# Performance work log

Hardware: AMD Instinct MI355X
Metric: run time of the kernel (lower is better)

Reference implementation:

```python
import jax, jax.numpy as jnp
import numpy as np

d_model = 512


def setup_inputs() -> dict:
    key = jax.random.key(0)
    k1, k2, k3, k4 = jax.random.split(key, 4)
    B, T, d_k = 8, 2048, 64
    scale = 1.0 / np.sqrt(d_model)
    x = jax.random.normal(k1, (B, T, d_model), dtype=jnp.float32)
    Wk = jax.random.normal(k2, (d_model, d_k), dtype=jnp.float32) * scale
    Wq = jax.random.normal(k3, (d_model, d_k), dtype=jnp.float32) * scale
    Wv = jax.random.normal(k4, (d_model, d_k), dtype=jnp.float32) * scale
    return {"x": x, "Wk": Wk, "Wq": Wq, "Wv": Wv}


def reference(x, Wk, Wq, Wv):
    # x: [B,T,C]; W*: [C,d_k]  (torch Linear weight is [d_k,C]; we store transposed)
    k = jnp.einsum('btc,cd->btd', x, Wk)
    q = jnp.einsum('btc,cd->btd', x, Wq)
    v = jnp.einsum('btc,cd->btd', x, Wv)
    d_k = k.shape[-1]
    scores = jnp.einsum('bqd,bkd->bqk', q, k) / jnp.sqrt(jnp.float32(d_k))
    attn = jax.nn.softmax(scores, axis=-1)  # [B,T,T]
    return jnp.einsum('bqk,bkd->bqd', attn, v)
```

## Files before the change

kernel.cpp:

```cpp
#include <hip/hip_runtime.h>
#include <hip/hip_bf16.h>
#include <stdint.h>


typedef short bf16x8 __attribute__((ext_vector_type(8)));
typedef float f32x4 __attribute__((ext_vector_type(4)));

#define MFMA_BF16 __builtin_amdgcn_mfma_f32_16x16x32_bf16

__device__ __forceinline__ unsigned int pk2(float a, float b) {
    __hip_bfloat162 h = __float22bfloat162_rn(float2{a, b});
    union { __hip_bfloat162 h; unsigned int u; } r; r.h = h;
    return r.u;
}

__device__ __forceinline__ uint2 pack4_bf16(float a, float b, float c, float d) {
    uint2 r; r.x = pk2(a, b); r.y = pk2(c, d); return r;
}

__device__ __forceinline__ bf16x8 cvt8(f32x4 a, f32x4 b) {
    union { bf16x8 v; unsigned int u[4]; } r;
    r.u[0] = pk2(a[0], a[1]); r.u[1] = pk2(a[2], a[3]);
    r.u[2] = pk2(b[0], b[1]); r.u[3] = pk2(b[2], b[3]);
    return r.v;
}

__device__ __forceinline__ unsigned short bf1(float a) {
    __hip_bfloat16 h = __float2bfloat16(a);
    union { __hip_bfloat16 h; unsigned short u; } r; r.h = h;
    return r.u;
}

__global__ void wt_kernel(const float* __restrict__ Wq,
                          const float* __restrict__ Wk,
                          const float* __restrict__ Wv,
                          unsigned short* __restrict__ wt2)
{
    int id = blockIdx.x * 256 + threadIdx.x;
    int c    = id & 15;
    int quad = (id >> 4) & 3;
    int ks   = (id >> 6) & 15;
    int mt   = (id >> 10) & 3;
    int w    = id >> 12;
    const float* src = (w == 0) ? Wq : ((w == 1) ? Wk : Wv);
    const int n  = mt * 16 + c;
    const int k0 = ks * 32 + quad * 8;
    unsigned short* dst = wt2 + (size_t)id * 8;
    #pragma unroll
    for (int j = 0; j < 8; j++)
        dst[j] = bf1(src[(size_t)(k0 + j) * 64 + n]);
}

__global__ __launch_bounds__(256, 1) void proj_kernel(
    const float* __restrict__ x, const unsigned short* __restrict__ wt2,
    unsigned short* __restrict__ qg, unsigned short* __restrict__ kg2,
    unsigned short* __restrict__ vg2)
{
    __shared__ unsigned short xs[8192];

    const int tid  = threadIdx.x;
    const int lane = tid & 63;
    const int wave = tid >> 6;
    const int c    = lane & 15;
    const int quad = lane >> 4;
    const int tt   = blockIdx.x;
    const int t0   = tt * 16;

    const float* xb = x + (size_t)tt * 8192;
    #pragma unroll
    for (int t = 0; t < 4; t++) {
        int i = t * 256 + tid;
        f32x4 a = *(const f32x4*)(xb + (size_t)i * 8);
        f32x4 b = *(const f32x4*)(xb + (size_t)i * 8 + 4);
        int tok = i >> 6;
        int db  = i & 63;
        *(bf16x8*)(xs + db * 128 + ((tok ^ (db & 7)) * 8)) = cvt8(a, b);
    }
    __syncthreads();

    f32x4 acc[3];
    #pragma unroll
    for (int r = 0; r < 3; r++) acc[r] = f32x4{0.f, 0.f, 0.f, 0.f};

    const int fbase = wave * 3;
    #pragma unroll 4
    for (int ks = 0; ks < 16; ks++) {
        bf16x8 xf = *(const bf16x8*)(
            xs + ks * 512 + quad * 128 + ((c ^ ((ks * 4 + quad) & 7)) * 8));
        #pragma unroll
        for (int r = 0; r < 3; r++) {
            int f = fbase + r;
            bf16x8 wa = *(const bf16x8*)(wt2 + ((size_t)(f * 16 + ks) * 64 + lane) * 8);
            acc[r] = MFMA_BF16(wa, xf, acc[r], 0, 0, 0);
        }
    }

    const int b  = t0 >> 11;
    const int tb = t0 & 2047;

    #pragma unroll
    for (int r = 0; r < 3; r++) {
        const int f  = fbase + r;
        const int w  = f >> 2;
        const int mt = f & 3;
        if (w == 0) {
            unsigned short* base = qg + (size_t)(t0 + c) * 64;
            *(uint2*)(base + mt * 16 + quad * 4) =
                pack4_bf16(acc[r][0], acc[r][1], acc[r][2], acc[r][3]);
        } else if (w == 1) {
            const int g  = tb >> 4;
            const int h  = mt >> 1;
            const int qk = (mt & 1) * 2 + (quad >> 1);
            size_t chunk = (size_t)b * 16384 + ((size_t)(g * 2 + h) * 4 + qk) * 16 + c;
            *(uint2*)(kg2 + chunk * 8 + (quad & 1) * 4) =
                pack4_bf16(acc[r][0], acc[r][1], acc[r][2], acc[r][3]);
        } else {
            const int tk = tb + c;
            const int s  = tk >> 5;
            const int qv = (tk >> 3) & 3;
            const int j  = tk & 7;
            size_t chunk = (size_t)b * 16384 + ((size_t)(s * 4 + mt) * 4 + qv) * 16 + quad * 4;
            unsigned short* dst = vg2 + chunk * 8 + j;
            dst[0]  = bf1(acc[r][0]);
            dst[8]  = bf1(acc[r][1]);
            dst[16] = bf1(acc[r][2]);
            dst[24] = bf1(acc[r][3]);
        }
    }
}

__global__ __launch_bounds__(512, 2) void attn_kernel(
    const unsigned short* __restrict__ qg, const unsigned short* __restrict__ kg2,
    const unsigned short* __restrict__ vg2, float* __restrict__ out)
{
    __shared__ __align__(16) unsigned short pt[8][4][16 * 136];
    __shared__ float lbuf[8][4][16];
    float* obase = reinterpret_cast<float*>(&pt[0][0][0]);

    const int lane = threadIdx.x & 63;
    const int wave = threadIdx.x >> 6;
    const int c    = lane & 15;
    const int quad = lane >> 4;
    const int b    = blockIdx.x & 7;
    const int g    = blockIdx.x >> 3;
    const int tb   = b * 2048 + g * 64;

    unsigned short* ptw = &pt[wave][0][0];
    const unsigned short* kbase = kg2 + ((size_t)b * 16384 + lane) * 8;
    const unsigned short* vbase = vg2 + ((size_t)b * 16384 + lane) * 8;

    bf16x8 qA0 = *(const bf16x8*)(qg + (size_t)(tb + c) * 64 + quad * 8);
    bf16x8 qA1 = *(const bf16x8*)(qg + (size_t)(tb + c) * 64 + 32 + quad * 8);
    bf16x8 qB0 = *(const bf16x8*)(qg + (size_t)(tb + 16 + c) * 64 + quad * 8);
    bf16x8 qB1 = *(const bf16x8*)(qg + (size_t)(tb + 16 + c) * 64 + 32 + quad * 8);
    bf16x8 qC0 = *(const bf16x8*)(qg + (size_t)(tb + 32 + c) * 64 + quad * 8);
    bf16x8 qC1 = *(const bf16x8*)(qg + (size_t)(tb + 32 + c) * 64 + 32 + quad * 8);
    bf16x8 qD0 = *(const bf16x8*)(qg + (size_t)(tb + 48 + c) * 64 + quad * 8);
    bf16x8 qD1 = *(const bf16x8*)(qg + (size_t)(tb + 48 + c) * 64 + 32 + quad * 8);

    f32x4 oa0 = {0,0,0,0}, oa1 = {0,0,0,0}, oa2 = {0,0,0,0}, oa3 = {0,0,0,0};
    f32x4 ob0 = {0,0,0,0}, ob1 = {0,0,0,0}, ob2 = {0,0,0,0}, ob3 = {0,0,0,0};
    f32x4 oc0 = {0,0,0,0}, oc1 = {0,0,0,0}, oc2 = {0,0,0,0}, oc3 = {0,0,0,0};
    f32x4 od0 = {0,0,0,0}, od1 = {0,0,0,0}, od2 = {0,0,0,0}, od3 = {0,0,0,0};
    f32x4 laccA = {0,0,0,0}, laccB = {0,0,0,0};
    f32x4 laccC = {0,0,0,0}, laccD = {0,0,0,0};
    const float cexp = 0.18033688011112042f;

    for (int kt = wave * 2; kt < wave * 2 + 2; kt++) {
        const int key0 = kt * 128;
        const int g0   = key0 >> 4;
        const int s0   = key0 >> 5;
        const f32x4 z = {0,0,0,0};

        f32x4 stA[8], stB[8];
        #pragma unroll
        for (int mt = 0; mt < 8; mt++) {
            bf16x8 k0 = *(const bf16x8*)(kbase + (size_t)((g0 + mt) * 2    ) * 64 * 8);
            bf16x8 k1 = *(const bf16x8*)(kbase + (size_t)((g0 + mt) * 2 + 1) * 64 * 8);
            stA[mt] = MFMA_BF16(k0, qA0, z, 0, 0, 0);
            stA[mt] = MFMA_BF16(k1, qA1, stA[mt], 0, 0, 0);
            stB[mt] = MFMA_BF16(k0, qB0, z, 0, 0, 0);
            stB[mt] = MFMA_BF16(k1, qB1, stB[mt], 0, 0, 0);
        }

        asm volatile("" ::: "memory");
        #pragma unroll
        for (int mt = 0; mt < 8; mt++) {
            float p0 = __builtin_amdgcn_exp2f(stA[mt][0] * cexp);
            float p1 = __builtin_amdgcn_exp2f(stA[mt][1] * cexp);
            float p2 = __builtin_amdgcn_exp2f(stA[mt][2] * cexp);
            float p3 = __builtin_amdgcn_exp2f(stA[mt][3] * cexp);
            laccA[0] += p0; laccA[1] += p1; laccA[2] += p2; laccA[3] += p3;
            *(uint2*)(ptw + c * 136 + mt * 16 + quad * 4) = pack4_bf16(p0, p1, p2, p3);
        }
        #pragma unroll
        for (int mt = 0; mt < 8; mt++) {
            float p0 = __builtin_amdgcn_exp2f(stB[mt][0] * cexp);
            float p1 = __builtin_amdgcn_exp2f(stB[mt][1] * cexp);
            float p2 = __builtin_amdgcn_exp2f(stB[mt][2] * cexp);
            float p3 = __builtin_amdgcn_exp2f(stB[mt][3] * cexp);
            laccB[0] += p0; laccB[1] += p1; laccB[2] += p2; laccB[3] += p3;
            *(uint2*)(ptw + 2176 + c * 136 + mt * 16 + quad * 4) = pack4_bf16(p0, p1, p2, p3);
        }
        asm volatile("" ::: "memory");

        f32x4 stC[8], stD[8];
        #pragma unroll
        for (int mt = 0; mt < 8; mt++) {
            bf16x8 k0 = *(const bf16x8*)(kbase + (size_t)((g0 + mt) * 2    ) * 64 * 8);
            bf16x8 k1 = *(const bf16x8*)(kbase + (size_t)((g0 + mt) * 2 + 1) * 64 * 8);
            stC[mt] = MFMA_BF16(k0, qC0, z, 0, 0, 0);
            stC[mt] = MFMA_BF16(k1, qC1, stC[mt], 0, 0, 0);
            stD[mt] = MFMA_BF16(k0, qD0, z, 0, 0, 0);
            stD[mt] = MFMA_BF16(k1, qD1, stD[mt], 0, 0, 0);
        }

        bf16x8 va[2][4];
        #pragma unroll
        for (int mt = 0; mt < 4; mt++) {
            va[0][mt] = *(const bf16x8*)(vbase + (size_t)((s0    ) * 4 + mt) * 64 * 8);
            va[1][mt] = *(const bf16x8*)(vbase + (size_t)((s0 + 1) * 4 + mt) * 64 * 8);
        }

        asm volatile("" ::: "memory");
        #pragma unroll
        for (int mt = 0; mt < 8; mt++) {
            float p0 = __builtin_amdgcn_exp2f(stC[mt][0] * cexp);
            float p1 = __builtin_amdgcn_exp2f(stC[mt][1] * cexp);
            float p2 = __builtin_amdgcn_exp2f(stC[mt][2] * cexp);
            float p3 = __builtin_amdgcn_exp2f(stC[mt][3] * cexp);
            laccC[0] += p0; laccC[1] += p1; laccC[2] += p2; laccC[3] += p3;
            *(uint2*)(ptw + 2 * 2176 + c * 136 + mt * 16 + quad * 4) = pack4_bf16(p0, p1, p2, p3);
        }
        #pragma unroll
        for (int mt = 0; mt < 8; mt++) {
            float p0 = __builtin_amdgcn_exp2f(stD[mt][0] * cexp);
            float p1 = __builtin_amdgcn_exp2f(stD[mt][1] * cexp);
            float p2 = __builtin_amdgcn_exp2f(stD[mt][2] * cexp);
            float p3 = __builtin_amdgcn_exp2f(stD[mt][3] * cexp);
            laccD[0] += p0; laccD[1] += p1; laccD[2] += p2; laccD[3] += p3;
            *(uint2*)(ptw + 3 * 2176 + c * 136 + mt * 16 + quad * 4) = pack4_bf16(p0, p1, p2, p3);
        }
        asm volatile("" ::: "memory");

        #pragma unroll
        for (int ks = 0; ks < 4; ks++) {
            bf16x8 pbA = *(const bf16x8*)(ptw            + c * 136 + ks * 32 + quad * 8);
            bf16x8 pbB = *(const bf16x8*)(ptw +     2176 + c * 136 + ks * 32 + quad * 8);
            bf16x8 pbC = *(const bf16x8*)(ptw + 2 * 2176 + c * 136 + ks * 32 + quad * 8);
            bf16x8 pbD = *(const bf16x8*)(ptw + 3 * 2176 + c * 136 + ks * 32 + quad * 8);
            bf16x8 v0 = va[ks & 1][0], v1 = va[ks & 1][1];
            bf16x8 v2 = va[ks & 1][2], v3 = va[ks & 1][3];
            if (ks < 2) {
                #pragma unroll
                for (int mt = 0; mt < 4; mt++)
                    va[ks & 1][mt] =
                        *(const bf16x8*)(vbase + (size_t)((s0 + ks + 2) * 4 + mt) * 64 * 8);
            }
            oa0 = MFMA_BF16(v0, pbA, oa0, 0, 0, 0);
            oa1 = MFMA_BF16(v1, pbA, oa1, 0, 0, 0);
            oa2 = MFMA_BF16(v2, pbA, oa2, 0, 0, 0);
            oa3 = MFMA_BF16(v3, pbA, oa3, 0, 0, 0);
            ob0 = MFMA_BF16(v0, pbB, ob0, 0, 0, 0);
            ob1 = MFMA_BF16(v1, pbB, ob1, 0, 0, 0);
            ob2 = MFMA_BF16(v2, pbB, ob2, 0, 0, 0);
            ob3 = MFMA_BF16(v3, pbB, ob3, 0, 0, 0);
            oc0 = MFMA_BF16(v0, pbC, oc0, 0, 0, 0);
            oc1 = MFMA_BF16(v1, pbC, oc1, 0, 0, 0);
            oc2 = MFMA_BF16(v2, pbC, oc2, 0, 0, 0);
            oc3 = MFMA_BF16(v3, pbC, oc3, 0, 0, 0);
            od0 = MFMA_BF16(v0, pbD, od0, 0, 0, 0);
            od1 = MFMA_BF16(v1, pbD, od1, 0, 0, 0);
            od2 = MFMA_BF16(v2, pbD, od2, 0, 0, 0);
            od3 = MFMA_BF16(v3, pbD, od3, 0, 0, 0);
        }
        asm volatile("" ::: "memory");
    }

    float lA = (laccA[0] + laccA[1]) + (laccA[2] + laccA[3]);
    lA += __shfl_xor(lA, 16); lA += __shfl_xor(lA, 32);
    float lB = (laccB[0] + laccB[1]) + (laccB[2] + laccB[3]);
    lB += __shfl_xor(lB, 16); lB += __shfl_xor(lB, 32);
    float lC = (laccC[0] + laccC[1]) + (laccC[2] + laccC[3]);
    lC += __shfl_xor(lC, 16); lC += __shfl_xor(lC, 32);
    float lD = (laccD[0] + laccD[1]) + (laccD[2] + laccD[3]);
    lD += __shfl_xor(lD, 16); lD += __shfl_xor(lD, 32);
    if (quad == 0) {
        lbuf[wave][0][c] = lA; lbuf[wave][1][c] = lB;
        lbuf[wave][2][c] = lC; lbuf[wave][3][c] = lD;
    }

    __syncthreads();

    if (wave < 4) {
        float* o0 = obase + ((size_t)(wave * 4 + 0) * 16 + c) * 68 + quad * 4;
        float* o1 = obase + ((size_t)(wave * 4 + 1) * 16 + c) * 68 + quad * 4;
        float* o2 = obase + ((size_t)(wave * 4 + 2) * 16 + c) * 68 + quad * 4;
        float* o3 = obase + ((size_t)(wave * 4 + 3) * 16 + c) * 68 + quad * 4;
        *(f32x4*)(o0 +  0) = oa0; *(f32x4*)(o0 + 16) = oa1;
        *(f32x4*)(o0 + 32) = oa2; *(f32x4*)(o0 + 48) = oa3;
        *(f32x4*)(o1 +  0) = ob0; *(f32x4*)(o1 + 16) = ob1;
        *(f32x4*)(o1 + 32) = ob2; *(f32x4*)(o1 + 48) = ob3;
        *(f32x4*)(o2 +  0) = oc0; *(f32x4*)(o2 + 16) = oc1;
        *(f32x4*)(o2 + 32) = oc2; *(f32x4*)(o2 + 48) = oc3;
        *(f32x4*)(o3 +  0) = od0; *(f32x4*)(o3 + 16) = od1;
        *(f32x4*)(o3 + 32) = od2; *(f32x4*)(o3 + 48) = od3;
    }
    __syncthreads();

    if (wave >= 4) {
        const int p = wave - 4;
        float* o0 = obase + ((size_t)(p * 4 + 0) * 16 + c) * 68 + quad * 4;
        float* o1 = obase + ((size_t)(p * 4 + 1) * 16 + c) * 68 + quad * 4;
        float* o2 = obase + ((size_t)(p * 4 + 2) * 16 + c) * 68 + quad * 4;
        float* o3 = obase + ((size_t)(p * 4 + 3) * 16 + c) * 68 + quad * 4;
        #define ADDSTORE(ptr, off, reg) { f32x4 t = *(f32x4*)((ptr) + (off)); \
            t[0] += reg[0]; t[1] += reg[1]; t[2] += reg[2]; t[3] += reg[3];   \
            *(f32x4*)((ptr) + (off)) = t; }
        ADDSTORE(o0,  0, oa0); ADDSTORE(o0, 16, oa1);
        ADDSTORE(o0, 32, oa2); ADDSTORE(o0, 48, oa3);
        ADDSTORE(o1,  0, ob0); ADDSTORE(o1, 16, ob1);
        ADDSTORE(o1, 32, ob2); ADDSTORE(o1, 48, ob3);
        ADDSTORE(o2,  0, oc0); ADDSTORE(o2, 16, oc1);
        ADDSTORE(o2, 32, oc2); ADDSTORE(o2, 48, oc3);
        ADDSTORE(o3,  0, od0); ADDSTORE(o3, 16, od1);
        ADDSTORE(o3, 32, od2); ADDSTORE(o3, 48, od3);
        #undef ADDSTORE
    }
    __syncthreads();

    const int tid = threadIdx.x;
    const int row = tid >> 3;
    const int d0  = (tid & 7) * 8;
    const int qt  = row >> 4;
    const int r   = row & 15;
    float L = 0.f;
    #pragma unroll
    for (int w = 0; w < 8; w++) L += lbuf[w][qt][r];
    const float rl = 1.f / L;
    f32x4 Oa = {0,0,0,0}, Ob = {0,0,0,0};
    #pragma unroll
    for (int p = 0; p < 4; p++) {
        const float* src = obase + ((size_t)(p * 4 + qt) * 16 + r) * 68 + d0;
        f32x4 a   = *(const f32x4*)(src);
        f32x4 bfr = *(const f32x4*)(src + 4);
        Oa[0] += a[0]; Oa[1] += a[1]; Oa[2] += a[2]; Oa[3] += a[3];
        Ob[0] += bfr[0]; Ob[1] += bfr[1]; Ob[2] += bfr[2]; Ob[3] += bfr[3];
    }
    Oa[0] *= rl; Oa[1] *= rl; Oa[2] *= rl; Oa[3] *= rl;
    Ob[0] *= rl; Ob[1] *= rl; Ob[2] *= rl; Ob[3] *= rl;
    float* op = out + (size_t)(tb + row) * 64 + d0;
    *(f32x4*)op       = Oa;
    *(f32x4*)(op + 4) = Ob;
}

extern "C" void kernel_launch(void* const* d_in, const int* in_sizes, int n_in,
                              void* d_out, int out_size, void* d_ws, size_t ws_size,
                              hipStream_t stream)
{
    const float* x  = (const float*)d_in[0];
    const float* Wk = (const float*)d_in[1];
    const float* Wq = (const float*)d_in[2];
    const float* Wv = (const float*)d_in[3];
    float* out = (float*)d_out;

    char* ws = (char*)d_ws;
    unsigned short* qg  = (unsigned short*)(ws);
    unsigned short* kg2 = (unsigned short*)(ws + (2u << 20));
    unsigned short* vg2 = (unsigned short*)(ws + (4u << 20));
    unsigned short* wt2 = (unsigned short*)(ws + (6u << 20));

    hipLaunchKernelGGL(wt_kernel,   dim3(48),   dim3(256), 0, stream,
                       Wq, Wk, Wv, wt2);
    hipLaunchKernelGGL(proj_kernel, dim3(1024), dim3(256), 0, stream,
                       x, wt2, qg, kg2, vg2);
    hipLaunchKernelGGL(attn_kernel, dim3(256),  dim3(512), 0, stream,
                       qg, kg2, vg2, out);
}
```

Measured before the change: 109.3 us.

## Process 64 tokens per projection block to reuse weight fragments across subtiles

The projection kernel now handles 64 tokens per block instead of 16, with four 16-token subtiles per wave. Each weight fragment loaded from global memory is reused across all four subtiles, which cuts repeated weight loads and raises MFMA density. The cost is a 64KB shared-memory staging buffer, four times as many accumulators per thread, and only 256 blocks instead of 1024. That lower block count may leave many compute units underused during the projection.

```diff
diff --git a/kernel.cpp b/kernel.cpp
--- a/kernel.cpp
+++ b/kernel.cpp
@@ -56,7 +56,7 @@
     unsigned short* __restrict__ qg, unsigned short* __restrict__ kg2,
     unsigned short* __restrict__ vg2)
 {
-    __shared__ unsigned short xs[8192];
+    __shared__ unsigned short xs[32768];
 
     const int tid  = threadIdx.x;
     const int lane = tid & 63;
@@ -64,67 +64,79 @@
     const int c    = lane & 15;
     const int quad = lane >> 4;
     const int tt   = blockIdx.x;
-    const int t0   = tt * 16;
-
-    const float* xb = x + (size_t)tt * 8192;
-    #pragma unroll
-    for (int t = 0; t < 4; t++) {
+    const int t0   = tt * 64;
+
+    const float* xb = x + (size_t)tt * 32768;
+    #pragma unroll
+    for (int t = 0; t < 16; t++) {
         int i = t * 256 + tid;
         f32x4 a = *(const f32x4*)(xb + (size_t)i * 8);
         f32x4 b = *(const f32x4*)(xb + (size_t)i * 8 + 4);
         int tok = i >> 6;
         int db  = i & 63;
-        *(bf16x8*)(xs + db * 128 + ((tok ^ (db & 7)) * 8)) = cvt8(a, b);
+        *(bf16x8*)(xs + ((size_t)db * 64 + (tok ^ (db & 7))) * 8) = cvt8(a, b);
     }
     __syncthreads();
 
-    f32x4 acc[3];
-    #pragma unroll
-    for (int r = 0; r < 3; r++) acc[r] = f32x4{0.f, 0.f, 0.f, 0.f};
+    f32x4 acc[3][4];
+    #pragma unroll
+    for (int r = 0; r < 3; r++)
+        #pragma unroll
+        for (int st = 0; st < 4; st++) acc[r][st] = f32x4{0.f, 0.f, 0.f, 0.f};
 
     const int fbase = wave * 3;
-    #pragma unroll 4
+    #pragma unroll 2
     for (int ks = 0; ks < 16; ks++) {
-        bf16x8 xf = *(const bf16x8*)(
-            xs + ks * 512 + quad * 128 + ((c ^ ((ks * 4 + quad) & 7)) * 8));
-        #pragma unroll
-        for (int r = 0; r < 3; r++) {
-            int f = fbase + r;
-            bf16x8 wa = *(const bf16x8*)(wt2 + ((size_t)(f * 16 + ks) * 64 + lane) * 8);
-            acc[r] = MFMA_BF16(wa, xf, acc[r], 0, 0, 0);
-        }
-    }
-
-    const int b  = t0 >> 11;
-    const int tb = t0 & 2047;
+        bf16x8 wa[3];
+        #pragma unroll
+        for (int r = 0; r < 3; r++)
+            wa[r] = *(const bf16x8*)(
+                wt2 + ((size_t)((fbase + r) * 16 + ks) * 64 + lane) * 8);
+        const int sw = c ^ ((ks & 1) * 4 + quad);
+        const unsigned short* xrow = xs + ((size_t)(ks * 4 + quad) * 64 + sw) * 8;
+        #pragma unroll
+        for (int st = 0; st < 4; st++) {
+            bf16x8 xf = *(const bf16x8*)(xrow + (size_t)st * 16 * 8);
+            #pragma unroll
+            for (int r = 0; r < 3; r++)
+                acc[r][st] = MFMA_BF16(wa[r], xf, acc[r][st], 0, 0, 0);
+        }
+    }
+
+    const int b = t0 >> 11;
 
     #pragma unroll
     for (int r = 0; r < 3; r++) {
         const int f  = fbase + r;
         const int w  = f >> 2;
         const int mt = f & 3;
-        if (w == 0) {
-            unsigned short* base = qg + (size_t)(t0 + c) * 64;
-            *(uint2*)(base + mt * 16 + quad * 4) =
-                pack4_bf16(acc[r][0], acc[r][1], acc[r][2], acc[r][3]);
-        } else if (w == 1) {
-            const int g  = tb >> 4;
-            const int h  = mt >> 1;
-            const int qk = (mt & 1) * 2 + (quad >> 1);
-            size_t chunk = (size_t)b * 16384 + ((size_t)(g * 2 + h) * 4 + qk) * 16 + c;
-            *(uint2*)(kg2 + chunk * 8 + (quad & 1) * 4) =
-                pack4_bf16(acc[r][0], acc[r][1], acc[r][2], acc[r][3]);
-        } else {
-            const int tk = tb + c;
-            const int s  = tk >> 5;
-            const int qv = (tk >> 3) & 3;
-            const int j  = tk & 7;
-            size_t chunk = (size_t)b * 16384 + ((size_t)(s * 4 + mt) * 4 + qv) * 16 + quad * 4;
-            unsigned short* dst = vg2 + chunk * 8 + j;
-            dst[0]  = bf1(acc[r][0]);
-            dst[8]  = bf1(acc[r][1]);
-            dst[16] = bf1(acc[r][2]);
-            dst[24] = bf1(acc[r][3]);
+        #pragma unroll
+        for (int st = 0; st < 4; st++) {
+            const int ts = t0 + st * 16;
+            const int tb = ts & 2047;
+            if (w == 0) {
+                unsigned short* base = qg + (size_t)(ts + c) * 64;
+                *(uint2*)(base + mt * 16 + quad * 4) =
+                    pack4_bf16(acc[r][st][0], acc[r][st][1], acc[r][st][2], acc[r][st][3]);
+            } else if (w == 1) {
+                const int g  = tb >> 4;
+                const int h  = mt >> 1;
+                const int qk = (mt & 1) * 2 + (quad >> 1);
+                size_t chunk = (size_t)b * 16384 + ((size_t)(g * 2 + h) * 4 + qk) * 16 + c;
+                *(uint2*)(kg2 + chunk * 8 + (quad & 1) * 4) =
+                    pack4_bf16(acc[r][st][0], acc[r][st][1], acc[r][st][2], acc[r][st][3]);
+            } else {
+                const int tk = tb + c;
+                const int s  = tk >> 5;
+                const int qv = (tk >> 3) & 3;
+                const int j  = tk & 7;
+                size_t chunk = (size_t)b * 16384 + ((size_t)(s * 4 + mt) * 4 + qv) * 16 + quad * 4;
+                unsigned short* dst = vg2 + chunk * 8 + j;
+                dst[0]  = bf1(acc[r][st][0]);
+                dst[8]  = bf1(acc[r][st][1]);
+                dst[16] = bf1(acc[r][st][2]);
+                dst[24] = bf1(acc[r][st][3]);
+            }
         }
     }
 }
@@ -372,7 +384,7 @@
 
     hipLaunchKernelGGL(wt_kernel,   dim3(48),   dim3(256), 0, stream,
                        Wq, Wk, Wv, wt2);
-    hipLaunchKernelGGL(proj_kernel, dim3(1024), dim3(256), 0, stream,
+    hipLaunchKernelGGL(proj_kernel, dim3(256),  dim3(256), 0, stream,
                        x, wt2, qg, kg2, vg2);
     hipLaunchKernelGGL(attn_kernel, dim3(256),  dim3(512), 0, stream,
                        qg, kg2, vg2, out);
```

Result: faster. 106.3 us (-2.8%).
